# Optimization experiments

Hardware: AMD Instinct MI355X
Metric: run time of the kernel (lower is better)

The kernel has to match this reference:

```python
import jax, jax.numpy as jnp
import numpy as np

HIDDEN_DIM = 1024
NUM_HEADS = 16
HEAD_DIM = HIDDEN_DIM // NUM_HEADS


def setup_inputs() -> dict:
    key = jax.random.key(0)
    ks = jax.random.split(key, 9)
    s = 1.0 / np.sqrt(HIDDEN_DIM)
    x = jax.random.normal(ks[0], (2, 2048, HIDDEN_DIM), dtype=jnp.float32)
    Wq = jax.random.uniform(ks[1], (HIDDEN_DIM, HIDDEN_DIM), jnp.float32, -s, s)
    bq = jax.random.uniform(ks[2], (HIDDEN_DIM,), jnp.float32, -s, s)
    Wk = jax.random.uniform(ks[3], (HIDDEN_DIM, HIDDEN_DIM), jnp.float32, -s, s)
    bk = jax.random.uniform(ks[4], (HIDDEN_DIM,), jnp.float32, -s, s)
    Wv = jax.random.uniform(ks[5], (HIDDEN_DIM, HIDDEN_DIM), jnp.float32, -s, s)
    bv = jax.random.uniform(ks[6], (HIDDEN_DIM,), jnp.float32, -s, s)
    Wo = jax.random.uniform(ks[7], (HIDDEN_DIM, HIDDEN_DIM), jnp.float32, -s, s)
    bo = jax.random.uniform(ks[8], (HIDDEN_DIM,), jnp.float32, -s, s)
    return {"x": x, "Wq": Wq, "bq": bq, "Wk": Wk, "bk": bk,
            "Wv": Wv, "bv": bv, "Wo": Wo, "bo": bo}


def reference(x, Wq, bq, Wk, bk, Wv, bv, Wo, bo):
    B, M, D = x.shape
    H, Dh = NUM_HEADS, HEAD_DIM
    # projections -> [B, H, M, Dh]
    def split_heads(t):
        return t.reshape(B, M, H, Dh).transpose(0, 2, 1, 3)
    q = split_heads(x @ Wq.T + bq)
    k = split_heads(x @ Wk.T + bk)
    v = split_heads(x @ Wv.T + bv)
    scores = jnp.einsum('bhmd,bhnd->bhmn', q, k) / np.sqrt(Dh).astype(np.float32)
    # multiplicative diagonal-zero mask: zero the diagonal of the score matrix
    diag_zero = 1.0 - jnp.eye(M, dtype=scores.dtype)  # [M, M]
    scores = scores * diag_zero
    attn = jax.nn.softmax(scores, axis=-1)
    context = jnp.einsum('bhmn,bhnd->bhmd', attn, v)
    context = context.transpose(0, 2, 1, 3).reshape(B, M, D)
    return context @ Wo.T + bo
```

## Files before the change

kernel.cpp:

```cpp
#include <hip/hip_runtime.h>
#include <stdint.h>

typedef _Float16 f16;
typedef __attribute__((ext_vector_type(8))) _Float16 f16x8;
typedef __attribute__((ext_vector_type(4))) _Float16 f16x4;
typedef __attribute__((ext_vector_type(4))) float f32x4;

#define HD 1024
#define NH 16
#define DH 64
#define BB 2
#define MM 2048
#define BH (BB*NH)
#define MT (BB*MM)

__device__ __forceinline__ void gl_lds16(const f16* g, f16* l) {
    __builtin_amdgcn_global_load_lds((const __attribute__((address_space(1))) uint32_t*)g,
                                     (__attribute__((address_space(3))) uint32_t*)l, 16, 0, 0);
}

__device__ __forceinline__ float fexp2(float x) {
    float r; asm("v_exp_f32 %0, %1" : "=v"(r) : "v"(x)); return r;
}

__global__ void cvt_all(const float* __restrict__ x,  const float* __restrict__ wq,
                        const float* __restrict__ wk, const float* __restrict__ wv,
                        const float* __restrict__ wo, f16* __restrict__ dst) {
    const int XN4 = MT * HD / 4;
    const int WN4 = HD * HD / 4;
    int i = blockIdx.x * blockDim.x + threadIdx.x;
    if (i >= XN4 + 4 * WN4) return;
    const float* s; int off;
    if (i < XN4) { s = x; off = i; }
    else {
        int k = i - XN4, wsel = k >> 18;
        off = k & (WN4 - 1);
        s = wsel == 0 ? wq : wsel == 1 ? wk : wsel == 2 ? wv : wo;
    }
    float4 v = ((const float4*)s)[off];
    f16x4 h;
    h[0] = (f16)v.x; h[1] = (f16)v.y; h[2] = (f16)v.z; h[3] = (f16)v.w;
    ((f16x4*)dst)[i] = h;
}

template<int MODE>
__global__ __launch_bounds__(256, 3) void gemm_m97(const f16* __restrict__ A,
                                                   const f16* __restrict__ W,
                                                   const float* __restrict__ b0,
                                                   const float* __restrict__ b1,
                                                   const float* __restrict__ b2,
                                                   f16* __restrict__ oh,
                                                   float* __restrict__ of) {
    __shared__ f16 As[128 * 32];
    __shared__ f16 Bs[128 * 32];
    const int bn = blockIdx.x, bm = blockIdx.y;
    const int t = threadIdx.x, w = t >> 6, lane = t & 63;
    const int wr = w >> 1, wc = w & 1, lr = lane & 15, lg = lane >> 4;
    f32x4 acc[4][4] = {};

    const int srow = w * 16 + (lane >> 2);
    const int schunk = lane & 3;
    const f16* Ab = A + (size_t)(bm * 128) * HD;
    const f16* Wb = W + (size_t)(bn * 128) * HD;
    f16* Asw = As + w * 512;
    f16* Bsw = Bs + w * 512;

    #pragma unroll
    for (int i = 0; i < 2; i++) {
        int r = i * 64 + srow;
        int gc = ((schunk ^ ((r >> 1) & 3)) * 8);
        gl_lds16(Ab + (size_t)r * HD + gc, Asw + i * 2048);
        gl_lds16(Wb + (size_t)r * HD + gc, Bsw + i * 2048);
    }

    for (int k0 = 0;;) {
        __syncthreads();
        f16x8 af[4], bf[4];
        #pragma unroll
        for (int i = 0; i < 4; i++) {
            int ra = wr * 64 + i * 16 + lr;
            af[i] = *(const f16x8*)(As + ra * 32 + ((lg ^ ((ra >> 1) & 3)) * 8));
            int rb = wc * 64 + i * 16 + lr;
            bf[i] = *(const f16x8*)(Bs + rb * 32 + ((lg ^ ((rb >> 1) & 3)) * 8));
        }
        #pragma unroll
        for (int i = 0; i < 4; i++)
            #pragma unroll
            for (int j = 0; j < 4; j++)
                acc[i][j] = __builtin_amdgcn_mfma_f32_16x16x32_f16(af[i], bf[j], acc[i][j], 0, 0, 0);
        k0 += 32;
        if (k0 >= HD) break;
        __syncthreads();
        #pragma unroll
        for (int i = 0; i < 2; i++) {
            int r = i * 64 + srow;
            int gc = ((schunk ^ ((r >> 1) & 3)) * 8);
            gl_lds16(Ab + (size_t)r * HD + k0 + gc, Asw + i * 2048);
            gl_lds16(Wb + (size_t)r * HD + k0 + gc, Bsw + i * 2048);
        }
    }

    if (MODE == 0) {
        const int mat = bn >> 3;
        const float* bp = mat == 0 ? b0 : mat == 1 ? b1 : b2;
        f16* base = oh + (size_t)mat * BH * MM * DH;
        #pragma unroll
        for (int i = 0; i < 4; i++) {
            #pragma unroll
            for (int j = 0; j < 4; j++) {
                int n = bn * 128 + wc * 64 + j * 16 + lr;
                int nn = n & 1023, h = nn >> 6, dh = nn & 63;
                float bvv = bp[nn];
                int mg0 = bm * 128 + wr * 64 + i * 16 + lg * 4;
                int b = mg0 >> 11, mmr0 = mg0 & 2047;
                if (mat == 2) {
                    f16x4 o;
                    #pragma unroll
                    for (int r = 0; r < 4; r++) o[r] = (f16)(acc[i][j][r] + bvv);
                    *(f16x4*)(base + ((size_t)((b * NH + h) * DH + dh)) * MM + mmr0) = o;
                } else {
                    float sc = (mat == 0) ? 0.1803368801111204f : 1.0f;
                    #pragma unroll
                    for (int r = 0; r < 4; r++)
                        base[((size_t)((b * NH + h) * MM + mmr0 + r)) * DH + dh] =
                            (f16)((acc[i][j][r] + bvv) * sc);
                }
            }
        }
    } else {
        #pragma unroll
        for (int i = 0; i < 4; i++)
            #pragma unroll
            for (int j = 0; j < 4; j++) {
                int n = bn * 128 + wc * 64 + j * 16 + lr;
                float bvv = b0[n];
                #pragma unroll
                for (int r = 0; r < 4; r++) {
                    int mg = bm * 128 + wr * 64 + i * 16 + lg * 4 + r;
                    of[(size_t)mg * HD + n] = acc[i][j][r] + bvv;
                }
            }
    }
}

__global__ __launch_bounds__(256, 4) void attn_kernel(const f16* __restrict__ Q,
                                                      const f16* __restrict__ K,
                                                      const f16* __restrict__ Vt,
                                                      f16* __restrict__ ctx) {
    __shared__ f16 Kl[2][64][64];
    __shared__ f16 Vl[2][64][64];
    __shared__ f16 Pl[4][16][64];
    const int bid = blockIdx.x;
    const int xcd = bid & 7, idx = bid >> 3;
    const int bh = xcd * 4 + (idx >> 5);
    const int qblk = idx & 31;

    const int t = threadIdx.x, w = t >> 6, lane = t & 63;
    const int lr = lane & 15, lg = lane >> 4;
    const int q0 = qblk * 64 + w * 16;

    const f16* Qb = Q + (size_t)bh * MM * DH;
    const f16* Kb = K + (size_t)bh * MM * DH;
    const f16* Vb = Vt + (size_t)bh * DH * MM;

    const int srow = lane >> 3;
    const int sxc = ((lane & 7) ^ srow) * 8;

    f16x8 qfr[2];
    #pragma unroll
    for (int c = 0; c < 2; c++)
        qfr[c] = *(const f16x8*)(Qb + (size_t)(q0 + lr) * DH + c * 32 + lg * 8);

    f32x4 po[4] = {};
    float m_ = -1e30f, l_ = 0.f;
    const int sw = (lr & 7) * 8;
    f16* Pw = &Pl[w][0][0];

    #pragma unroll
    for (int i = 0; i < 2; i++) {
        int row = w * 16 + i * 8 + srow;
        gl_lds16(Kb + (size_t)row * DH + sxc, &Kl[0][w * 16 + i * 8][0]);
        gl_lds16(Vb + (size_t)row * MM + sxc, &Vl[0][w * 16 + i * 8][0]);
    }
    __syncthreads();

    for (int it = 0; it < 32; ++it) {
        const int j0 = it * 64;
        const int cur = it & 1;
        if (it < 31) {
            #pragma unroll
            for (int i = 0; i < 2; i++) {
                int row = w * 16 + i * 8 + srow;
                gl_lds16(Kb + (size_t)(j0 + 64 + row) * DH + sxc, &Kl[cur ^ 1][w * 16 + i * 8][0]);
                gl_lds16(Vb + (size_t)row * MM + j0 + 64 + sxc, &Vl[cur ^ 1][w * 16 + i * 8][0]);
            }
        }
        f32x4 sa[4] = {};
        #pragma unroll
        for (int f = 0; f < 4; f++) {
            const f16* kr = &Kl[cur][f * 16 + lr][0];
            f16x8 k0 = *(const f16x8*)(kr + ((lg * 8) ^ sw));
            f16x8 k1 = *(const f16x8*)(kr + ((32 + lg * 8) ^ sw));
            sa[f] = __builtin_amdgcn_mfma_f32_16x16x32_f16(k0, qfr[0], sa[f], 0, 0, 0);
            sa[f] = __builtin_amdgcn_mfma_f32_16x16x32_f16(k1, qfr[1], sa[f], 0, 0, 0);
        }
        if (it == qblk) {
            int q = q0 + lr;
            #pragma unroll
            for (int f = 0; f < 4; f++)
                #pragma unroll
                for (int r = 0; r < 4; r++)
                    if (q == j0 + f * 16 + lg * 4 + r) sa[f][r] = 0.f;
        }
        float pmax = sa[0][0];
        #pragma unroll
        for (int f = 0; f < 4; f++)
            #pragma unroll
            for (int r = 0; r < 4; r++) pmax = fmaxf(pmax, sa[f][r]);
        pmax = fmaxf(pmax, __shfl_xor(pmax, 16));
        pmax = fmaxf(pmax, __shfl_xor(pmax, 32));
        if (__any(pmax > m_ + 8.f)) {
            float mn = fmaxf(m_, pmax);
            float al = fexp2(m_ - mn);
            m_ = mn; l_ *= al;
            #pragma unroll
            for (int df = 0; df < 4; df++)
                #pragma unroll
                for (int r = 0; r < 4; r++) po[df][r] *= al;
        }
        float rs = 0.f;
        #pragma unroll
        for (int f = 0; f < 4; f++) {
            f16x4 pk;
            #pragma unroll
            for (int r = 0; r < 4; r++) {
                float p = fexp2(sa[f][r] - m_);
                rs += p; pk[r] = (f16)p;
            }
            *(f16x4*)(Pw + lr * 64 + ((f * 16 + lg * 4) ^ sw)) = pk;
        }
        rs += __shfl_xor(rs, 16);
        rs += __shfl_xor(rs, 32);
        l_ += rs;
        asm volatile("s_waitcnt lgkmcnt(0)" ::: "memory");
        f16x8 pf0 = *(const f16x8*)(Pw + lr * 64 + ((lg * 8) ^ sw));
        f16x8 pf1 = *(const f16x8*)(Pw + lr * 64 + ((32 + lg * 8) ^ sw));
        #pragma unroll
        for (int df = 0; df < 4; df++) {
            const f16* vr = &Vl[cur][df * 16 + lr][0];
            f16x8 v0 = *(const f16x8*)(vr + ((lg * 8) ^ sw));
            f16x8 v1 = *(const f16x8*)(vr + ((32 + lg * 8) ^ sw));
            po[df] = __builtin_amdgcn_mfma_f32_16x16x32_f16(v0, pf0, po[df], 0, 0, 0);
            po[df] = __builtin_amdgcn_mfma_f32_16x16x32_f16(v1, pf1, po[df], 0, 0, 0);
        }
        __syncthreads();
    }
    const int b = bh >> 4, h = bh & 15;
    const float inv = 1.f / l_;
    f16* cp = ctx + ((size_t)(b * MM + q0 + lr)) * HD + h * DH;
    #pragma unroll
    for (int df = 0; df < 4; df++) {
        f16x4 o;
        #pragma unroll
        for (int r = 0; r < 4; r++) o[r] = (f16)(po[df][r] * inv);
        *(f16x4*)(cp + df * 16 + lg * 4) = o;
    }
}

extern "C" void kernel_launch(void* const* d_in, const int* in_sizes, int n_in,
                              void* d_out, int out_size, void* d_ws, size_t ws_size,
                              hipStream_t stream) {
    const float* x  = (const float*)d_in[0];
    const float* Wq = (const float*)d_in[1];
    const float* bq = (const float*)d_in[2];
    const float* Wk = (const float*)d_in[3];
    const float* bk = (const float*)d_in[4];
    const float* Wv = (const float*)d_in[5];
    const float* bv = (const float*)d_in[6];
    const float* Wo = (const float*)d_in[7];
    const float* bo = (const float*)d_in[8];
    float* out = (float*)d_out;

    f16* xh  = (f16*)d_ws;
    f16* wqh = xh  + (size_t)MT * HD;
    f16* woh = wqh + (size_t)3 * HD * HD;
    f16* Qh  = woh + (size_t)HD * HD;
    f16* ctxh= Qh  + (size_t)3 * BH * MM * DH;

    const int total4 = MT * HD / 4 + HD * HD;
    cvt_all<<<(total4 + 255) / 256, 256, 0, stream>>>(x, Wq, Wk, Wv, Wo, xh);

    gemm_m97<0><<<dim3(3 * HD / 128, MT / 128), 256, 0, stream>>>(xh, wqh, bq, bk, bv, Qh, nullptr);

    attn_kernel<<<1024, 256, 0, stream>>>(Qh, Qh + (size_t)BH * MM * DH,
                                          Qh + (size_t)2 * BH * MM * DH, ctxh);

    gemm_m97<1><<<dim3(HD / 128, MT / 128), 256, 0, stream>>>(ctxh, woh, bo, nullptr, nullptr,
                                                              nullptr, out);
}
```

Measured before the change: 130.1 us.

## Software-pipeline QK^T one tile ahead in attention and remap GEMM blocks per XCD

The attention loop now computes the next tile's QK^T scores while softmax and PV run on the current tile. K is prefetched two tiles ahead and V one tile ahead, and MFMA sections run under raised s_setprio. The GEMMs use a 1D grid with an XCD-aware block mapping for the QKV projection, which should improve L2 reuse of weight tiles. Smaller changes are packed f16 conversion via cvt_pkrtz and a tree-shaped max reduction. These add register pressure from the extra score accumulators, and the wrap-around prefetch loads at the end do redundant work.

```diff
diff --git a/kernel.cpp b/kernel.cpp
--- a/kernel.cpp
+++ b/kernel.cpp
@@ -4,6 +4,7 @@
 typedef _Float16 f16;
 typedef __attribute__((ext_vector_type(8))) _Float16 f16x8;
 typedef __attribute__((ext_vector_type(4))) _Float16 f16x4;
+typedef __attribute__((ext_vector_type(2))) __fp16 fp16x2;
 typedef __attribute__((ext_vector_type(4))) float f32x4;
 
 #define HD 1024
@@ -53,7 +54,10 @@
                                                    float* __restrict__ of) {
     __shared__ f16 As[128 * 32];
     __shared__ f16 Bs[128 * 32];
-    const int bn = blockIdx.x, bm = blockIdx.y;
+    const int bid = blockIdx.x;
+    int bn, bm;
+    if (MODE == 0) { int xcd = bid & 7, r = bid >> 3; bn = xcd * 3 + (r >> 5); bm = r & 31; }
+    else           { bn = bid & 7; bm = bid >> 3; }
     const int t = threadIdx.x, w = t >> 6, lane = t & 63;
     const int wr = w >> 1, wc = w & 1, lr = lane & 15, lg = lane >> 4;
     f32x4 acc[4][4] = {};
@@ -165,6 +169,7 @@
 
     const int srow = lane >> 3;
     const int sxc = ((lane & 7) ^ srow) * 8;
+    const int lds_r = w * 16;
 
     f16x8 qfr[2];
     #pragma unroll
@@ -178,45 +183,61 @@
 
     #pragma unroll
     for (int i = 0; i < 2; i++) {
-        int row = w * 16 + i * 8 + srow;
-        gl_lds16(Kb + (size_t)row * DH + sxc, &Kl[0][w * 16 + i * 8][0]);
-        gl_lds16(Vb + (size_t)row * MM + sxc, &Vl[0][w * 16 + i * 8][0]);
+        int row = lds_r + i * 8 + srow;
+        gl_lds16(Kb + (size_t)row * DH + sxc, &Kl[0][lds_r + i * 8][0]);
+        gl_lds16(Vb + (size_t)row * MM + sxc, &Vl[0][lds_r + i * 8][0]);
     }
     __syncthreads();
-
+    f32x4 sa[4] = {};
+    #pragma unroll
+    for (int f = 0; f < 4; f++) {
+        const f16* kr = &Kl[0][f * 16 + lr][0];
+        f16x8 k0 = *(const f16x8*)(kr + ((lg * 8) ^ sw));
+        f16x8 k1 = *(const f16x8*)(kr + ((32 + lg * 8) ^ sw));
+        sa[f] = __builtin_amdgcn_mfma_f32_16x16x32_f16(k0, qfr[0], sa[f], 0, 0, 0);
+        sa[f] = __builtin_amdgcn_mfma_f32_16x16x32_f16(k1, qfr[1], sa[f], 0, 0, 0);
+    }
+    #pragma unroll
+    for (int i = 0; i < 2; i++) {
+        int row = lds_r + i * 8 + srow;
+        gl_lds16(Kb + (size_t)(64 + row) * DH + sxc, &Kl[1][lds_r + i * 8][0]);
+    }
+    __syncthreads();
+
+    #pragma unroll 2
     for (int it = 0; it < 32; ++it) {
-        const int j0 = it * 64;
-        const int cur = it & 1;
-        if (it < 31) {
-            #pragma unroll
-            for (int i = 0; i < 2; i++) {
-                int row = w * 16 + i * 8 + srow;
-                gl_lds16(Kb + (size_t)(j0 + 64 + row) * DH + sxc, &Kl[cur ^ 1][w * 16 + i * 8][0]);
-                gl_lds16(Vb + (size_t)row * MM + j0 + 64 + sxc, &Vl[cur ^ 1][w * 16 + i * 8][0]);
-            }
-        }
-        f32x4 sa[4] = {};
+        const int cb = it & 1;
+        const int jv = ((it + 1) & 31) * 64;
+        const int jk = ((it + 2) & 31) * 64;
+        #pragma unroll
+        for (int i = 0; i < 2; i++) {
+            int row = lds_r + i * 8 + srow;
+            gl_lds16(Vb + (size_t)row * MM + jv + sxc, &Vl[cb ^ 1][lds_r + i * 8][0]);
+            gl_lds16(Kb + (size_t)(jk + row) * DH + sxc, &Kl[cb][lds_r + i * 8][0]);
+        }
+        f32x4 sn[4] = {};
+        __builtin_amdgcn_s_setprio(1);
         #pragma unroll
         for (int f = 0; f < 4; f++) {
-            const f16* kr = &Kl[cur][f * 16 + lr][0];
+            const f16* kr = &Kl[cb ^ 1][f * 16 + lr][0];
             f16x8 k0 = *(const f16x8*)(kr + ((lg * 8) ^ sw));
             f16x8 k1 = *(const f16x8*)(kr + ((32 + lg * 8) ^ sw));
-            sa[f] = __builtin_amdgcn_mfma_f32_16x16x32_f16(k0, qfr[0], sa[f], 0, 0, 0);
-            sa[f] = __builtin_amdgcn_mfma_f32_16x16x32_f16(k1, qfr[1], sa[f], 0, 0, 0);
-        }
+            sn[f] = __builtin_amdgcn_mfma_f32_16x16x32_f16(k0, qfr[0], sn[f], 0, 0, 0);
+            sn[f] = __builtin_amdgcn_mfma_f32_16x16x32_f16(k1, qfr[1], sn[f], 0, 0, 0);
+        }
+        __builtin_amdgcn_s_setprio(0);
         if (it == qblk) {
             int q = q0 + lr;
             #pragma unroll
             for (int f = 0; f < 4; f++)
                 #pragma unroll
                 for (int r = 0; r < 4; r++)
-                    if (q == j0 + f * 16 + lg * 4 + r) sa[f][r] = 0.f;
-        }
-        float pmax = sa[0][0];
-        #pragma unroll
-        for (int f = 0; f < 4; f++)
-            #pragma unroll
-            for (int r = 0; r < 4; r++) pmax = fmaxf(pmax, sa[f][r]);
+                    if (q == it * 64 + f * 16 + lg * 4 + r) sa[f][r] = 0.f;
+        }
+        float pmax = fmaxf(fmaxf(fmaxf(sa[0][0], sa[0][1]), fmaxf(sa[0][2], sa[0][3])),
+                           fmaxf(fmaxf(sa[1][0], sa[1][1]), fmaxf(sa[1][2], sa[1][3])));
+        pmax = fmaxf(pmax, fmaxf(fmaxf(fmaxf(sa[2][0], sa[2][1]), fmaxf(sa[2][2], sa[2][3])),
+                                 fmaxf(fmaxf(sa[3][0], sa[3][1]), fmaxf(sa[3][2], sa[3][3]))));
         pmax = fmaxf(pmax, __shfl_xor(pmax, 16));
         pmax = fmaxf(pmax, __shfl_xor(pmax, 32));
         if (__any(pmax > m_ + 8.f)) {
@@ -231,12 +252,13 @@
         float rs = 0.f;
         #pragma unroll
         for (int f = 0; f < 4; f++) {
-            f16x4 pk;
-            #pragma unroll
-            for (int r = 0; r < 4; r++) {
-                float p = fexp2(sa[f][r] - m_);
-                rs += p; pk[r] = (f16)p;
-            }
+            float p0 = fexp2(sa[f][0] - m_), p1 = fexp2(sa[f][1] - m_);
+            float p2 = fexp2(sa[f][2] - m_), p3 = fexp2(sa[f][3] - m_);
+            rs += (p0 + p1) + (p2 + p3);
+            fp16x2 lo = __builtin_amdgcn_cvt_pkrtz(p0, p1);
+            fp16x2 hi = __builtin_amdgcn_cvt_pkrtz(p2, p3);
+            uint2 pr; pr.x = __builtin_bit_cast(uint32_t, lo); pr.y = __builtin_bit_cast(uint32_t, hi);
+            f16x4 pk = __builtin_bit_cast(f16x4, pr);
             *(f16x4*)(Pw + lr * 64 + ((f * 16 + lg * 4) ^ sw)) = pk;
         }
         rs += __shfl_xor(rs, 16);
@@ -245,14 +267,18 @@
         asm volatile("s_waitcnt lgkmcnt(0)" ::: "memory");
         f16x8 pf0 = *(const f16x8*)(Pw + lr * 64 + ((lg * 8) ^ sw));
         f16x8 pf1 = *(const f16x8*)(Pw + lr * 64 + ((32 + lg * 8) ^ sw));
+        __builtin_amdgcn_s_setprio(1);
         #pragma unroll
         for (int df = 0; df < 4; df++) {
-            const f16* vr = &Vl[cur][df * 16 + lr][0];
+            const f16* vr = &Vl[cb][df * 16 + lr][0];
             f16x8 v0 = *(const f16x8*)(vr + ((lg * 8) ^ sw));
             f16x8 v1 = *(const f16x8*)(vr + ((32 + lg * 8) ^ sw));
             po[df] = __builtin_amdgcn_mfma_f32_16x16x32_f16(v0, pf0, po[df], 0, 0, 0);
             po[df] = __builtin_amdgcn_mfma_f32_16x16x32_f16(v1, pf1, po[df], 0, 0, 0);
         }
+        __builtin_amdgcn_s_setprio(0);
+        #pragma unroll
+        for (int f = 0; f < 4; f++) sa[f] = sn[f];
         __syncthreads();
     }
     const int b = bh >> 4, h = bh & 15;
@@ -290,11 +316,10 @@
     const int total4 = MT * HD / 4 + HD * HD;
     cvt_all<<<(total4 + 255) / 256, 256, 0, stream>>>(x, Wq, Wk, Wv, Wo, xh);
 
-    gemm_m97<0><<<dim3(3 * HD / 128, MT / 128), 256, 0, stream>>>(xh, wqh, bq, bk, bv, Qh, nullptr);
+    gemm_m97<0><<<768, 256, 0, stream>>>(xh, wqh, bq, bk, bv, Qh, nullptr);
 
     attn_kernel<<<1024, 256, 0, stream>>>(Qh, Qh + (size_t)BH * MM * DH,
                                           Qh + (size_t)2 * BH * MM * DH, ctxh);
 
-    gemm_m97<1><<<dim3(HD / 128, MT / 128), 256, 0, stream>>>(ctxh, woh, bo, nullptr, nullptr,
-                                                              nullptr, out);
-}
+    gemm_m97<1><<<256, 256, 0, stream>>>(ctxh, woh, bo, nullptr, nullptr, nullptr, out);
+}
```

Result: no change. 131.5 us (+1.1%).
